# Performance work log

Hardware: AMD Instinct MI355X
Metric: run time of the kernel (lower is better)

The kernel has to match this reference:

```python
import jax, jax.numpy as jnp
import numpy as np

K = 3
EPS = 1e-16

def setup_inputs() -> dict:
    key = jax.random.key(0)
    k1, k2, k3 = jax.random.split(key, 3)
    x = jax.random.normal(k1, (4096, 256), dtype=jnp.float32)
    pos_l = jax.random.normal(k2, (4096, 3), dtype=jnp.float32)
    pos_h = jax.random.normal(k3, (16384, 3), dtype=jnp.float32)
    return {"x": x, "pos_l": pos_l, "pos_h": pos_h}

def reference(x, pos_l, pos_h):
    # Squared pairwise distances [N_h, N_l] via expansion (GEMM-friendly)
    d2 = (jnp.sum(pos_h * pos_h, axis=1)[:, None]
          - 2.0 * pos_h @ pos_l.T
          + jnp.sum(pos_l * pos_l, axis=1)[None, :])
    # k nearest coarse neighbors per fine point
    _, idx = jax.lax.top_k(-d2, K)                      # idx: [N_h, K]
    # Recompute exact squared distances for selected neighbors (matches PyG knn_interpolate)
    diff = pos_h[:, None, :] - pos_l[idx]               # [N_h, K, D]
    d2_sel = jnp.sum(diff * diff, axis=-1)              # [N_h, K]
    w = 1.0 / jnp.clip(d2_sel, EPS)                     # inverse-distance weights
    feats = x[idx]                                      # [N_h, K, F]
    y = jnp.sum(feats * w[:, :, None], axis=1) / jnp.sum(w, axis=1, keepdims=True)
    return y
```

## Files before the change

kernel.cpp:

```cpp
#include <hip/hip_runtime.h>
#include <math.h>

#define NL    4096
#define NH    16384
#define NF4   64
#define BLK   1024
#define NW    16
#define FPB   64
#define PERW  (NL / NW)
#define TOPM  6

typedef float v16f __attribute__((ext_vector_type(16)));
typedef float v2f  __attribute__((ext_vector_type(2)));

__device__ __forceinline__ unsigned int med3u(unsigned int a, unsigned int b,
                                              unsigned int c)
{
  unsigned int d;
  asm("v_med3_u32 %0, %1, %2, %3" : "=v"(d) : "v"(a), "v"(b), "v"(c));
  return d;
}
__device__ __forceinline__ unsigned int minu(unsigned int a, unsigned int b)
{
  unsigned int d;
  asm("v_min_u32 %0, %1, %2" : "=v"(d) : "v"(a), "v"(b));
  return d;
}
__device__ __forceinline__ void ins6(unsigned int k,
    unsigned int& b0, unsigned int& b1, unsigned int& b2,
    unsigned int& b3, unsigned int& b4, unsigned int& b5)
{
  const unsigned int n0 = minu(b0, k);
  const unsigned int n1 = med3u(k, b0, b1);
  const unsigned int n2 = med3u(k, b1, b2);
  const unsigned int n3 = med3u(k, b2, b3);
  const unsigned int n4 = med3u(k, b3, b4);
  const unsigned int n5 = med3u(k, b4, b5);
  b0 = n0; b1 = n1; b2 = n2; b3 = n3; b4 = n4; b5 = n5;
}

__device__ __forceinline__ void lexins3(float d, int j,
    float& b0, float& b1, float& b2, int& i0, int& i1, int& i2)
{
  bool s2 = (d < b2) || ((d == b2) && (j < i2));
  b2 = s2 ? d : b2;  i2 = s2 ? j : i2;
  bool s1 = (b2 < b1) || ((b2 == b1) && (i2 < i1));
  float tf = b1; int ti = i1;
  b1 = s1 ? b2 : b1;  i1 = s1 ? i2 : i1;
  b2 = s1 ? tf : b2;  i2 = s1 ? ti : i2;
  bool s0 = (b1 < b0) || ((b1 == b0) && (i1 < i0));
  tf = b0; ti = i0;
  b0 = s0 ? b1 : b0;  i0 = s0 ? i1 : i0;
  b1 = s0 ? tf : b1;  i1 = s0 ? ti : i1;
}

__device__ __forceinline__ v2f dist2_pk(v2f lx, v2f ly, v2f lz, v2f ll,
                                        v2f h00, v2f h11, v2f h22, v2f hhh,
                                        v2f m22)
{
  v2f d;
  asm("v_pk_mul_f32 %0, %1, %2\n\t"
      "v_pk_fma_f32 %0, %3, %4, %0\n\t"
      "v_pk_fma_f32 %0, %5, %6, %0\n\t"
      "v_pk_fma_f32 %0, %0, %7, %8\n\t"
      "v_pk_add_f32 %0, %0, %9"
      : "=&v"(d)
      : "v"(h00), "s"(lx), "v"(h11), "s"(ly), "v"(h22), "s"(lz),
        "v"(m22), "v"(hhh), "s"(ll));
  return d;
}

__global__ __launch_bounds__(256)
void prep_soa_kernel(const float* __restrict__ pos_l, float* __restrict__ cand)
{
  const int i = blockIdx.x * 256 + threadIdx.x;
  const float l0 = pos_l[i * 3 + 0];
  const float l1 = pos_l[i * 3 + 1];
  const float l2 = pos_l[i * 3 + 2];
  const float ll = __fadd_rn(__fadd_rn(__fmul_rn(l0, l0), __fmul_rn(l1, l1)),
                             __fmul_rn(l2, l2));
  cand[i]          = l0;
  cand[NL + i]     = l1;
  cand[2 * NL + i] = l2;
  cand[3 * NL + i] = ll;
}

__global__ __launch_bounds__(BLK)
void knn_interp_kernel(const float* __restrict__ x,
                       const float* __restrict__ pos_l,
                       const float* __restrict__ pos_h,
                       const float* __restrict__ cand,
                       float* __restrict__ out)
{
  __shared__ unsigned int pk_[NW * FPB * TOPM];
  __shared__ float wn[FPB * 3];
  __shared__ int   sj[FPB * 3];

  const int tid  = threadIdx.x;
  const int lane = tid & 63;
  const int wv   = __builtin_amdgcn_readfirstlane(tid >> 6);
  const int fg   = blockIdx.x * FPB + lane;

  const float h0 = pos_h[fg * 3 + 0];
  const float h1 = pos_h[fg * 3 + 1];
  const float h2 = pos_h[fg * 3 + 2];
  const float hh = __fadd_rn(__fadd_rn(__fmul_rn(h0, h0), __fmul_rn(h1, h1)),
                             __fmul_rn(h2, h2));
  const v2f h00 = { h0, h0 }, h11 = { h1, h1 }, h22 = { h2, h2 };
  const v2f hhh = { hh, hh }, m22 = { -2.0f, -2.0f };

  unsigned int kmaskv;
  asm("v_mov_b32 %0, 0xfffff000" : "=v"(kmaskv));

  unsigned int a0 = ~0u, a1 = ~0u, a2 = ~0u, a3 = ~0u, a4 = ~0u, a5 = ~0u;
  unsigned int c0 = ~0u, c1 = ~0u, c2 = ~0u, c3 = ~0u, c4 = ~0u, c5 = ~0u;

  const int jbase = __builtin_amdgcn_readfirstlane(wv * PERW);

  for (int t = 0; t < PERW; t += 16) {
    v16f sx, sy, sz, sw;
    const float* p = cand + jbase + t;
    asm volatile("s_load_dwordx16 %0, %4, 0x0\n\t"
                 "s_load_dwordx16 %1, %4, 0x4000\n\t"
                 "s_load_dwordx16 %2, %4, 0x8000\n\t"
                 "s_load_dwordx16 %3, %4, 0xc000"
                 : "=&s"(sx), "=&s"(sy), "=&s"(sz), "=&s"(sw)
                 : "s"(p));
    asm volatile("s_waitcnt lgkmcnt(0)"
                 : "+s"(sx), "+s"(sy), "+s"(sz), "+s"(sw));

    #pragma unroll
    for (int pr = 0; pr < 8; ++pr) {
      const v2f lx = { sx[2 * pr], sx[2 * pr + 1] };
      const v2f ly = { sy[2 * pr], sy[2 * pr + 1] };
      const v2f lz = { sz[2 * pr], sz[2 * pr + 1] };
      const v2f lw = { sw[2 * pr], sw[2 * pr + 1] };
      const v2f d  = dist2_pk(lx, ly, lz, lw, h00, h11, h22, hhh, m22);
      const float dx0 = fmaxf(d.x, 0.0f);
      const float dy0 = fmaxf(d.y, 0.0f);
      const int j0 = jbase + t + 2 * pr;
      const int j1 = j0 + 1;
      unsigned int k0, k1;
      asm("v_and_or_b32 %0, %1, %2, %3"
          : "=v"(k0) : "v"(dx0), "v"(kmaskv), "s"(j0));
      asm("v_and_or_b32 %0, %1, %2, %3"
          : "=v"(k1) : "v"(dy0), "v"(kmaskv), "s"(j1));
      ins6(k0, a0, a1, a2, a3, a4, a5);
      ins6(k1, c0, c1, c2, c3, c4, c5);
    }
  }

  ins6(c0, a0, a1, a2, a3, a4, a5);
  ins6(c1, a0, a1, a2, a3, a4, a5);
  ins6(c2, a0, a1, a2, a3, a4, a5);
  ins6(c3, a0, a1, a2, a3, a4, a5);
  ins6(c4, a0, a1, a2, a3, a4, a5);
  ins6(c5, a0, a1, a2, a3, a4, a5);

  {
    const int s = (wv * FPB + lane) * TOPM;
    pk_[s + 0] = a0; pk_[s + 1] = a1; pk_[s + 2] = a2;
    pk_[s + 3] = a3; pk_[s + 4] = a4; pk_[s + 5] = a5;
  }
  __syncthreads();

  if (tid < FPB) {
    unsigned int m0 = ~0u, m1 = ~0u, m2 = ~0u, m3 = ~0u, m4 = ~0u, m5 = ~0u;
    for (int w = 0; w < NW; ++w) {
      const int s = (w * FPB + tid) * TOPM;
      #pragma unroll
      for (int q = 0; q < TOPM; ++q)
        ins6(pk_[s + q], m0, m1, m2, m3, m4, m5);
    }

    const float b_hh = hh;
    float e0 = INFINITY, e1 = INFINITY, e2 = INFINITY;
    int   i0 = 0x7fffffff, i1 = 0x7fffffff, i2 = 0x7fffffff;
    const unsigned int mk[TOPM] = { m0, m1, m2, m3, m4, m5 };
    #pragma unroll
    for (int q = 0; q < TOPM; ++q) {
      const int j = (int)(mk[q] & 0xFFFu);
      const float lx = cand[j];
      const float ly = cand[NL + j];
      const float lz = cand[2 * NL + j];
      const float ll = cand[3 * NL + j];
      const float dot = __fmaf_rn(h2, lz, __fmaf_rn(h1, ly, __fmul_rn(h0, lx)));
      const float d2  = __fadd_rn(__fsub_rn(b_hh, __fmul_rn(2.0f, dot)), ll);
      lexins3(d2, j, e0, e1, e2, i0, i1, i2);
    }

    const int fm = blockIdx.x * FPB + tid;
    const float H0 = pos_h[fm * 3 + 0];
    const float H1 = pos_h[fm * 3 + 1];
    const float H2 = pos_h[fm * 3 + 2];
    float wk[3];
    int   jk[3] = { i0, i1, i2 };
    #pragma unroll
    for (int k = 0; k < 3; ++k) {
      const int j = jk[k];
      const float dx = __fsub_rn(H0, pos_l[j * 3 + 0]);
      const float dy = __fsub_rn(H1, pos_l[j * 3 + 1]);
      const float dz = __fsub_rn(H2, pos_l[j * 3 + 2]);
      float d2 = __fadd_rn(__fadd_rn(__fmul_rn(dx, dx), __fmul_rn(dy, dy)),
                           __fmul_rn(dz, dz));
      d2 = fmaxf(d2, 1e-16f);
      wk[k] = __frcp_rn(d2);
    }
    const float W  = __fadd_rn(__fadd_rn(wk[0], wk[1]), wk[2]);
    const float rW = __frcp_rn(W);
    #pragma unroll
    for (int k = 0; k < 3; ++k) {
      wn[tid * 3 + k] = wk[k] * rW;
      sj[tid * 3 + k] = jk[k];
    }
  }
  __syncthreads();

  const float4* __restrict__ x4   = (const float4*)x;
  float4* __restrict__       out4 = (float4*)out;
  #pragma unroll
  for (int i = 0; i < (FPB * NF4) / BLK; ++i) {
    const int task = tid + i * BLK;
    const int f    = task >> 6;
    const int cc   = task & 63;
    const int j0 = sj[f * 3 + 0], j1 = sj[f * 3 + 1], j2 = sj[f * 3 + 2];
    const float w0 = wn[f * 3 + 0], w1 = wn[f * 3 + 1], w2 = wn[f * 3 + 2];
    const float4 xa = x4[j0 * NF4 + cc];
    const float4 xb = x4[j1 * NF4 + cc];
    const float4 xc = x4[j2 * NF4 + cc];
    float4 r;
    r.x = xa.x * w0 + xb.x * w1 + xc.x * w2;
    r.y = xa.y * w0 + xb.y * w1 + xc.y * w2;
    r.z = xa.z * w0 + xb.z * w1 + xc.z * w2;
    r.w = xa.w * w0 + xb.w * w1 + xc.w * w2;
    out4[(blockIdx.x * FPB + f) * NF4 + cc] = r;
  }
}

extern "C" void kernel_launch(void* const* d_in, const int* in_sizes, int n_in,
                              void* d_out, int out_size, void* d_ws, size_t ws_size,
                              hipStream_t stream)
{
  const float* x     = (const float*)d_in[0];
  const float* pos_l = (const float*)d_in[1];
  const float* pos_h = (const float*)d_in[2];
  float* out  = (float*)d_out;
  float* cand = (float*)d_ws;

  hipLaunchKernelGGL(prep_soa_kernel, dim3(NL / 256), dim3(256), 0, stream,
                     pos_l, cand);
  hipLaunchKernelGGL(knn_interp_kernel, dim3(NH / FPB), dim3(BLK), 0, stream,
                     x, pos_l, pos_h, cand, out);
}
```

Measured before the change: 99.38 us.

## Double-buffer scalar candidate loads, shrink shortlist to 5, use signed keys

The candidate loop now double-buffers 8-wide scalar loads, so the next chunk is in flight while the current one is evaluated, instead of a blocking 16-wide load per iteration. The per-lane shortlist shrinks from 6 to 5 entries, cutting one med3 per insertion and reducing shared memory and the merge work. Keys are now compared as signed ints with the fmax clamp removed, relying on negative distances sorting first. This risks slightly different tie and negative-distance handling and a shortlist margin that is less robust to approximate-key ties.

```diff
diff --git a/kernel.cpp b/kernel.cpp
--- a/kernel.cpp
+++ b/kernel.cpp
@@ -8,35 +8,33 @@
 #define NW    16
 #define FPB   64
 #define PERW  (NL / NW)
-#define TOPM  6
-
-typedef float v16f __attribute__((ext_vector_type(16)));
-typedef float v2f  __attribute__((ext_vector_type(2)));
-
-__device__ __forceinline__ unsigned int med3u(unsigned int a, unsigned int b,
-                                              unsigned int c)
-{
-  unsigned int d;
-  asm("v_med3_u32 %0, %1, %2, %3" : "=v"(d) : "v"(a), "v"(b), "v"(c));
+#define TOPM  5
+#define SENT  0x7fffffff
+
+typedef float v8f __attribute__((ext_vector_type(8)));
+typedef float v2f __attribute__((ext_vector_type(2)));
+
+__device__ __forceinline__ int med3i(int a, int b, int c)
+{
+  int d;
+  asm("v_med3_i32 %0, %1, %2, %3" : "=v"(d) : "v"(a), "v"(b), "v"(c));
   return d;
 }
-__device__ __forceinline__ unsigned int minu(unsigned int a, unsigned int b)
-{
-  unsigned int d;
-  asm("v_min_u32 %0, %1, %2" : "=v"(d) : "v"(a), "v"(b));
+__device__ __forceinline__ int mini(int a, int b)
+{
+  int d;
+  asm("v_min_i32 %0, %1, %2" : "=v"(d) : "v"(a), "v"(b));
   return d;
 }
-__device__ __forceinline__ void ins6(unsigned int k,
-    unsigned int& b0, unsigned int& b1, unsigned int& b2,
-    unsigned int& b3, unsigned int& b4, unsigned int& b5)
-{
-  const unsigned int n0 = minu(b0, k);
-  const unsigned int n1 = med3u(k, b0, b1);
-  const unsigned int n2 = med3u(k, b1, b2);
-  const unsigned int n3 = med3u(k, b2, b3);
-  const unsigned int n4 = med3u(k, b3, b4);
-  const unsigned int n5 = med3u(k, b4, b5);
-  b0 = n0; b1 = n1; b2 = n2; b3 = n3; b4 = n4; b5 = n5;
+__device__ __forceinline__ void ins5(int k, int& b0, int& b1, int& b2,
+                                     int& b3, int& b4)
+{
+  const int n0 = mini(b0, k);
+  const int n1 = med3i(k, b0, b1);
+  const int n2 = med3i(k, b1, b2);
+  const int n3 = med3i(k, b2, b3);
+  const int n4 = med3i(k, b3, b4);
+  b0 = n0; b1 = n1; b2 = n2; b3 = n3; b4 = n4;
 }
 
 __device__ __forceinline__ void lexins3(float d, int j,
@@ -70,6 +68,17 @@
   return d;
 }
 
+#define LOADCH(X, Y, Z, W, P)                                   \
+  asm volatile("s_load_dwordx8 %0, %4, 0x0\n\t"                 \
+               "s_load_dwordx8 %1, %4, 0x4000\n\t"              \
+               "s_load_dwordx8 %2, %4, 0x8000\n\t"              \
+               "s_load_dwordx8 %3, %4, 0xc000"                  \
+               : "=&s"(X), "=&s"(Y), "=&s"(Z), "=&s"(W)         \
+               : "s"(P))
+#define WAITCH(X, Y, Z, W)                                      \
+  asm volatile("s_waitcnt lgkmcnt(0)"                           \
+               : "+s"(X), "+s"(Y), "+s"(Z), "+s"(W))
+
 __global__ __launch_bounds__(256)
 void prep_soa_kernel(const float* __restrict__ pos_l, float* __restrict__ cand)
 {
@@ -92,7 +101,7 @@
                        const float* __restrict__ cand,
                        float* __restrict__ out)
 {
-  __shared__ unsigned int pk_[NW * FPB * TOPM];
+  __shared__ int   pk_[NW * FPB * TOPM];
   __shared__ float wn[FPB * 3];
   __shared__ int   sj[FPB * 3];
 
@@ -112,80 +121,80 @@
   unsigned int kmaskv;
   asm("v_mov_b32 %0, 0xfffff000" : "=v"(kmaskv));
 
-  unsigned int a0 = ~0u, a1 = ~0u, a2 = ~0u, a3 = ~0u, a4 = ~0u, a5 = ~0u;
-  unsigned int c0 = ~0u, c1 = ~0u, c2 = ~0u, c3 = ~0u, c4 = ~0u, c5 = ~0u;
+  int a0 = SENT, a1 = SENT, a2 = SENT, a3 = SENT, a4 = SENT;
+  int c0 = SENT, c1 = SENT, c2 = SENT, c3 = SENT, c4 = SENT;
 
   const int jbase = __builtin_amdgcn_readfirstlane(wv * PERW);
 
-  for (int t = 0; t < PERW; t += 16) {
-    v16f sx, sy, sz, sw;
-    const float* p = cand + jbase + t;
-    asm volatile("s_load_dwordx16 %0, %4, 0x0\n\t"
-                 "s_load_dwordx16 %1, %4, 0x4000\n\t"
-                 "s_load_dwordx16 %2, %4, 0x8000\n\t"
-                 "s_load_dwordx16 %3, %4, 0xc000"
-                 : "=&s"(sx), "=&s"(sy), "=&s"(sz), "=&s"(sw)
-                 : "s"(p));
-    asm volatile("s_waitcnt lgkmcnt(0)"
-                 : "+s"(sx), "+s"(sy), "+s"(sz), "+s"(sw));
-
-    #pragma unroll
-    for (int pr = 0; pr < 8; ++pr) {
-      const v2f lx = { sx[2 * pr], sx[2 * pr + 1] };
-      const v2f ly = { sy[2 * pr], sy[2 * pr + 1] };
-      const v2f lz = { sz[2 * pr], sz[2 * pr + 1] };
-      const v2f lw = { sw[2 * pr], sw[2 * pr + 1] };
-      const v2f d  = dist2_pk(lx, ly, lz, lw, h00, h11, h22, hhh, m22);
-      const float dx0 = fmaxf(d.x, 0.0f);
-      const float dy0 = fmaxf(d.y, 0.0f);
-      const int j0 = jbase + t + 2 * pr;
-      const int j1 = j0 + 1;
-      unsigned int k0, k1;
-      asm("v_and_or_b32 %0, %1, %2, %3"
-          : "=v"(k0) : "v"(dx0), "v"(kmaskv), "s"(j0));
-      asm("v_and_or_b32 %0, %1, %2, %3"
-          : "=v"(k1) : "v"(dy0), "v"(kmaskv), "s"(j1));
-      ins6(k0, a0, a1, a2, a3, a4, a5);
-      ins6(k1, c0, c1, c2, c3, c4, c5);
-    }
-  }
-
-  ins6(c0, a0, a1, a2, a3, a4, a5);
-  ins6(c1, a0, a1, a2, a3, a4, a5);
-  ins6(c2, a0, a1, a2, a3, a4, a5);
-  ins6(c3, a0, a1, a2, a3, a4, a5);
-  ins6(c4, a0, a1, a2, a3, a4, a5);
-  ins6(c5, a0, a1, a2, a3, a4, a5);
+#define EVAL8(X, Y, Z, W, JB)                                              \
+  do {                                                                     \
+    _Pragma("unroll")                                                      \
+    for (int pr = 0; pr < 4; ++pr) {                                       \
+      const v2f lx = { X[2 * pr], X[2 * pr + 1] };                         \
+      const v2f ly = { Y[2 * pr], Y[2 * pr + 1] };                         \
+      const v2f lz = { Z[2 * pr], Z[2 * pr + 1] };                         \
+      const v2f lw = { W[2 * pr], W[2 * pr + 1] };                         \
+      const v2f d  = dist2_pk(lx, ly, lz, lw, h00, h11, h22, hhh, m22);    \
+      const int j0 = (JB) + 2 * pr;                                        \
+      const int j1 = j0 + 1;                                               \
+      int k0, k1;                                                          \
+      asm("v_and_or_b32 %0, %1, %2, %3"                                    \
+          : "=v"(k0) : "v"(d.x), "v"(kmaskv), "s"(j0));                    \
+      asm("v_and_or_b32 %0, %1, %2, %3"                                    \
+          : "=v"(k1) : "v"(d.y), "v"(kmaskv), "s"(j1));                    \
+      ins5(k0, a0, a1, a2, a3, a4);                                        \
+      ins5(k1, c0, c1, c2, c3, c4);                                        \
+    }                                                                      \
+  } while (0)
+
+  {
+    v8f ax_, ay_, az_, aw_, bx_, by_, bz_, bw_;
+    LOADCH(ax_, ay_, az_, aw_, cand + jbase);
+    for (int t = 0; t < PERW; t += 16) {
+      WAITCH(ax_, ay_, az_, aw_);
+      LOADCH(bx_, by_, bz_, bw_, cand + jbase + t + 8);
+      EVAL8(ax_, ay_, az_, aw_, jbase + t);
+      WAITCH(bx_, by_, bz_, bw_);
+      LOADCH(ax_, ay_, az_, aw_, cand + jbase + t + 16);
+      EVAL8(bx_, by_, bz_, bw_, jbase + t + 8);
+    }
+  }
+#undef EVAL8
+
+  ins5(c0, a0, a1, a2, a3, a4);
+  ins5(c1, a0, a1, a2, a3, a4);
+  ins5(c2, a0, a1, a2, a3, a4);
+  ins5(c3, a0, a1, a2, a3, a4);
+  ins5(c4, a0, a1, a2, a3, a4);
 
   {
     const int s = (wv * FPB + lane) * TOPM;
     pk_[s + 0] = a0; pk_[s + 1] = a1; pk_[s + 2] = a2;
-    pk_[s + 3] = a3; pk_[s + 4] = a4; pk_[s + 5] = a5;
+    pk_[s + 3] = a3; pk_[s + 4] = a4;
   }
   __syncthreads();
 
   if (tid < FPB) {
-    unsigned int m0 = ~0u, m1 = ~0u, m2 = ~0u, m3 = ~0u, m4 = ~0u, m5 = ~0u;
+    int m0 = SENT, m1 = SENT, m2 = SENT, m3 = SENT, m4 = SENT;
     for (int w = 0; w < NW; ++w) {
       const int s = (w * FPB + tid) * TOPM;
       #pragma unroll
       for (int q = 0; q < TOPM; ++q)
-        ins6(pk_[s + q], m0, m1, m2, m3, m4, m5);
-    }
-
-    const float b_hh = hh;
+        ins5(pk_[s + q], m0, m1, m2, m3, m4);
+    }
+
     float e0 = INFINITY, e1 = INFINITY, e2 = INFINITY;
     int   i0 = 0x7fffffff, i1 = 0x7fffffff, i2 = 0x7fffffff;
-    const unsigned int mk[TOPM] = { m0, m1, m2, m3, m4, m5 };
+    const int mk[TOPM] = { m0, m1, m2, m3, m4 };
     #pragma unroll
     for (int q = 0; q < TOPM; ++q) {
-      const int j = (int)(mk[q] & 0xFFFu);
+      const int j = mk[q] & 0xFFF;
       const float lx = cand[j];
       const float ly = cand[NL + j];
       const float lz = cand[2 * NL + j];
       const float ll = cand[3 * NL + j];
       const float dot = __fmaf_rn(h2, lz, __fmaf_rn(h1, ly, __fmul_rn(h0, lx)));
-      const float d2  = __fadd_rn(__fsub_rn(b_hh, __fmul_rn(2.0f, dot)), ll);
+      const float d2  = __fadd_rn(__fsub_rn(hh, __fmul_rn(2.0f, dot)), ll);
       lexins3(d2, j, e0, e1, e2, i0, i1, i2);
     }
 
```

Result: faster. 91.98 us (-7.4%).
